# Performance work log

Measured on AMD Instinct MI355X. Metric: run time of the kernel, lower is better.

## Reference

```python
import jax, jax.numpy as jnp
import numpy as np

B, T, D, H, LORA = 4, 1024, 1024, 16, 64
HD = D // H
BLOCK_ID, N_BLOCKS = 6, 12


def _ln(x, w, b, eps=1e-5):
    m = x.mean(-1, keepdims=True)
    v = ((x - m) ** 2).mean(-1, keepdims=True)
    return (x - m) * jax.lax.rsqrt(v + eps) * w + b


def _lora(z, a, b, l):
    return l + jnp.tanh(z @ a.T) @ b.T


def setup_inputs() -> dict:
    key = jax.random.key(0)
    ks = iter(jax.random.split(key, 64))
    rn = lambda shape, s: jax.random.normal(next(ks), shape, jnp.float32) * s
    inp = {}
    inp['x'] = rn((B, T, D), 1.0)
    r1 = 1.0 - BLOCK_ID / N_BLOCKS
    i = np.arange(D)
    inp['xw'] = jnp.asarray(1.0 - (i / D) ** r1, jnp.float32)
    for nm in ('rW', 'kW', 'vW', 'gW'):
        inp[nm] = rn((D, D), 0.02)
    for p in ('r', 'k', 'v', 'g', 'd'):
        inp[p + '_la'] = rn((LORA, D), 0.001)
        inp[p + '_lb'] = rn((D, LORA), 0.001)
        inp[p + '_ll'] = rn((D,), 1.0)
    inp['ln_w'] = jnp.full((HD,), ((1 + BLOCK_ID) / N_BLOCKS) ** 0.7, jnp.float32)
    inp['ln_b'] = jnp.zeros((HD,), jnp.float32)
    inp['oW'] = rn((D, D), 0.02)
    inp['init_state'] = rn((H, HD, HD), 1.0)
    r0 = BLOCK_ID / (N_BLOCKS - 1)
    ih = i % HD
    inp['u'] = jnp.asarray(r0 * (1 - ih / (D - 1)) + np.remainder(0.1 * (ih + 1), 3.0), jnp.float32)
    return inp


def reference(x, xw, rW, kW, vW, gW, r_la, r_lb, r_ll, k_la, k_lb, k_ll,
              v_la, v_lb, v_ll, g_la, g_lb, g_ll, d_la, d_lb, d_ll,
              ln_w, ln_b, oW, init_state, u):
    b, t, d = x.shape
    h = init_state.shape[0]
    hd = d // h
    # token shift: xx[t] = x[t-1], xx[0] = 0
    xx = jnp.concatenate([jnp.zeros_like(x[:, :1]), x[:, :-1]], axis=1)
    dx = xx - x
    lerpx = x + dx * xw
    r = (x + dx * _lora(lerpx, r_la, r_lb, r_ll)) @ rW.T
    k = (x + dx * _lora(lerpx, k_la, k_lb, k_ll)) @ kW.T
    v = (x + dx * _lora(lerpx, v_la, v_lb, v_ll)) @ vW.T
    g = (x + dx * _lora(lerpx, g_la, g_lb, g_ll)) @ gW.T
    w = jnp.exp(-jnp.exp(_lora(x + dx * _lora(lerpx, d_la, d_lb, d_ll), d_la, d_lb, d_ll)))
    # [B,T,D] -> [T,B,H,hd] for the time scan
    split = lambda z: z.reshape(b, t, h, hd).transpose(1, 0, 2, 3)
    rs, ws, ks, vs = split(r), split(w), split(k), split(v)
    uh = u.reshape(h, hd)
    st0 = jnp.broadcast_to(init_state, (b, h, hd, hd))

    def step(st, inp):
        rt, wt, kt, vt = inp
        kv = jnp.einsum('bhi,bhj->bhij', kt, vt)      # outer product
        y = jnp.einsum('bhi,bhij->bhj', rt, st + uh[None, :, :, None] * kv)
        return wt[..., None] * st + kv, y             # diag(w) @ S + kv

    st1, ys = jax.lax.scan(step, st0, (rs, ws, ks, vs))  # ys: [T,B,H,hd]
    o = jax.nn.silu(g.reshape(b, t, h, hd)) * _ln(ys.transpose(1, 0, 2, 3), ln_w, ln_b)
    return o.reshape(b, t, d) @ oW.T, st1
```

## Files before the change

### kernel.cpp

```cpp
#include <hip/hip_runtime.h>
#include <hip/hip_bf16.h>

typedef unsigned short u16;
typedef unsigned int u32;
typedef __attribute__((ext_vector_type(2))) float f32x2;
typedef __attribute__((ext_vector_type(4))) float f32x4;
typedef __attribute__((ext_vector_type(4))) u32 u32x4;
typedef __attribute__((ext_vector_type(8))) short s16x8;

#define AS1 __attribute__((address_space(1)))
#define AS3 __attribute__((address_space(3)))

#define NB 4
#define TTOK 1024
#define DD 1024
#define NH 16
#define HD 64
#define MT 4096
#define NCH 16
#define CLEN 64

struct Ptr8 { u16* p[8]; };
struct CPtr8 { const u16* p[8]; };

static __device__ __forceinline__ float b2f(u16 u) {
  union { unsigned int u; float f; } c; c.u = ((unsigned int)u) << 16; return c.f;
}
static __device__ __forceinline__ float ubit(u32 u) {
  union { u32 u; float f; } c; c.u = u; return c.f;
}
static __device__ __forceinline__ u16 f2b(float f) {
  union { float f; unsigned int u; } c; c.f = f;
  return (u16)((c.u + 0x7fffu + ((c.u >> 16) & 1u)) >> 16);
}
static __device__ __forceinline__ void gload16(const u16* g, u16* l) {
  __builtin_amdgcn_global_load_lds((const AS1 u32*)g, (AS3 u32*)l, 16, 0, 0);
}
static __device__ __forceinline__ int swz(int lin) {
  return lin ^ (((lin >> 9) & 3) << 5) ^ (((lin >> 7) & 1) << 4);
}

__global__ __launch_bounds__(256) void convW(const float* __restrict__ s0, const float* __restrict__ s1,
                                             const float* __restrict__ s2, const float* __restrict__ s3,
                                             const float* __restrict__ s4, u16* __restrict__ dst) {
  long f = ((long)blockIdx.x * 256 + threadIdx.x) << 2;
  int sel = (int)(f >> 20);
  const float* s = sel == 0 ? s0 : sel == 1 ? s1 : sel == 2 ? s2 : sel == 3 ? s3 : s4;
  long off = f & 1048575;
  f32x4 v = *(const f32x4*)&s[off];
  ushort4 o; o.x = f2b(v[0]); o.y = f2b(v[1]); o.z = f2b(v[2]); o.w = f2b(v[3]);
  *(ushort4*)&dst[f] = o;
}

__global__ __launch_bounds__(256) void convLora(
    const float* a0, const float* a1, const float* a2, const float* a3, const float* a4,
    const float* b0, const float* b1, const float* b2, const float* b3, const float* b4,
    const float* l0, const float* l1, const float* l2, const float* l3, const float* l4,
    u16* __restrict__ laD, u16* __restrict__ lbD, float* __restrict__ llD) {
  long f = ((long)blockIdx.x * 256 + threadIdx.x) << 2;
  if (f < 327680) {
    int sel = (int)(f >> 16); long off = f & 65535;
    const float* s = sel == 0 ? a0 : sel == 1 ? a1 : sel == 2 ? a2 : sel == 3 ? a3 : a4;
    f32x4 v = *(const f32x4*)&s[off];
    ushort4 o; o.x = f2b(v[0]); o.y = f2b(v[1]); o.z = f2b(v[2]); o.w = f2b(v[3]);
    *(ushort4*)&laD[f] = o;
  } else if (f < 655360) {
    long g = f - 327680;
    int sel = (int)(g >> 16); long off = g & 65535;
    const float* s = sel == 0 ? b0 : sel == 1 ? b1 : sel == 2 ? b2 : sel == 3 ? b3 : b4;
    f32x4 v = *(const f32x4*)&s[off];
    ushort4 o; o.x = f2b(v[0]); o.y = f2b(v[1]); o.z = f2b(v[2]); o.w = f2b(v[3]);
    *(ushort4*)&lbD[g] = o;
  } else if (f < 660480) {
    long g = f - 655360;
    int sel = (int)(g >> 10); long off = g & 1023;
    const float* s = sel == 0 ? l0 : sel == 1 ? l1 : sel == 2 ? l2 : sel == 3 ? l3 : l4;
    *(f32x4*)&llD[g] = *(const f32x4*)&s[off];
  }
}

__global__ __launch_bounds__(256) void prep(const float* __restrict__ x, const float* __restrict__ xw,
                                            u16* __restrict__ lerpx, u16* __restrict__ xB,
                                            u16* __restrict__ dxB) {
  long f = ((long)blockIdx.x * 256 + threadIdx.x) << 2;
  int d = (int)(f & (DD - 1));
  int m = (int)(f >> 10);
  int t = m & (TTOK - 1);
  f32x4 xv = *(const f32x4*)&x[f];
  f32x4 xm = {};
  if (t > 0) xm = *(const f32x4*)&x[f - DD];
  f32x4 xwv = *(const f32x4*)&xw[d];
  f32x4 dx = xm - xv;
  f32x4 lp = xv + dx * xwv;
  ushort4 o; o.x = f2b(lp[0]); o.y = f2b(lp[1]); o.z = f2b(lp[2]); o.w = f2b(lp[3]);
  *(ushort4*)&lerpx[f] = o;
  ushort4 ox; ox.x = f2b(xv[0]); ox.y = f2b(xv[1]); ox.z = f2b(xv[2]); ox.w = f2b(xv[3]);
  *(ushort4*)&xB[f] = ox;
  ushort4 od; od.x = f2b(dx[0]); od.y = f2b(dx[1]); od.z = f2b(dx[2]); od.w = f2b(dx[3]);
  *(ushort4*)&dxB[f] = od;
}

template<int BM, int BN, int EPI>
__launch_bounds__(256)
__global__ void gemm2(const u16* __restrict__ Ab, long sAz,
                      const u16* __restrict__ Bb, long sBz,
                      void* __restrict__ Ob, long sOz,
                      const float* __restrict__ llb,
                      const u16* __restrict__ xB,
                      const u16* __restrict__ dxB,
                      int M, int N, int K) {
  __shared__ __align__(16) u16 As[BM * 64];
  __shared__ __align__(16) u16 Bs[BN * 64];
  const int z = blockIdx.z;
  const u16* A = Ab + (long)z * sAz;
  const u16* Bw = Bb + (long)z * sBz;
  const int m0 = blockIdx.x * BM;
  const int n0 = blockIdx.y * BN;
  const int tid = threadIdx.x;
  const int l = tid & 63;
  const int wv = tid >> 6;
  constexpr int WM = BM / 2, WN = BN / 2;
  constexpr int FM = WM / 16, FN = WN / 16;
  const int wm0 = (wv >> 1) * WM, wn0 = (wv & 1) * WN;
  const int lrow = l & 15, lk = (l >> 4) * 8;
  constexpr int GA = BM / 32, GB = BN / 32;
  int gA[GA], gB[GB];
#pragma unroll
  for (int q = 0; q < GA; ++q) {
    int d = (q * 256 + tid) * 16;
    int bb = swz(d);
    gA[q] = (m0 + (bb >> 7)) * K + ((bb & 127) >> 1);
  }
#pragma unroll
  for (int q = 0; q < GB; ++q) {
    int d = (q * 256 + tid) * 16;
    int bb = swz(d);
    gB[q] = (n0 + (bb >> 7)) * K + ((bb & 127) >> 1);
  }
  int aOff[FM][2], bOff[FN][2];
#pragma unroll
  for (int m = 0; m < FM; ++m)
#pragma unroll
    for (int kk = 0; kk < 2; ++kk)
      aOff[m][kk] = swz(((wm0 + m * 16 + lrow) << 7) + (kk << 6) + (lk << 1));
#pragma unroll
  for (int n = 0; n < FN; ++n)
#pragma unroll
    for (int kk = 0; kk < 2; ++kk)
      bOff[n][kk] = swz(((wn0 + n * 16 + lrow) << 7) + (kk << 6) + (lk << 1));
  f32x4 acc[FM][FN] = {};
  for (int k0 = 0; k0 < K; k0 += 64) {
    __syncthreads();
#pragma unroll
    for (int q = 0; q < GA; ++q)
      gload16(&A[(long)gA[q] + k0], (u16*)((char*)As + (q * 256 + tid) * 16));
#pragma unroll
    for (int q = 0; q < GB; ++q)
      gload16(&Bw[(long)gB[q] + k0], (u16*)((char*)Bs + (q * 256 + tid) * 16));
    __syncthreads();
#pragma unroll
    for (int kk = 0; kk < 2; ++kk) {
      s16x8 af[FM], bfr[FN];
#pragma unroll
      for (int m = 0; m < FM; ++m) af[m] = *(const s16x8*)((const char*)As + aOff[m][kk]);
#pragma unroll
      for (int n = 0; n < FN; ++n) bfr[n] = *(const s16x8*)((const char*)Bs + bOff[n][kk]);
#pragma unroll
      for (int m = 0; m < FM; ++m)
#pragma unroll
        for (int n = 0; n < FN; ++n)
          acc[m][n] = __builtin_amdgcn_mfma_f32_16x16x32_bf16(af[m], bfr[n], acc[m][n], 0, 0, 0);
    }
  }
#pragma unroll
  for (int m = 0; m < FM; ++m) {
#pragma unroll
    for (int n = 0; n < FN; ++n) {
      const int j = n0 + wn0 + n * 16 + lrow;
#pragma unroll
      for (int q = 0; q < 4; ++q) {
        const int i = m0 + wm0 + m * 16 + (l >> 4) * 4 + q;
        const long off = (long)i * N + j;
        float v = acc[m][n][q];
        if constexpr (EPI == 0) {
          ((float*)Ob + (long)z * sOz)[off] = v;
        } else if constexpr (EPI == 1) {
          ((u16*)Ob + (long)z * sOz)[off] = f2b(tanhf(v));
        } else if constexpr (EPI == 2) {
          float val = b2f(xB[off]) + b2f(dxB[off]) * (llb[(long)z * N + j] + v);
          ((u16*)Ob + (long)z * sOz)[off] = f2b(val);
        } else if constexpr (EPI == 3) {
          ((float*)Ob + (long)z * sOz)[off] = expf(-expf(llb[j] + v));
        } else {
          ((u16*)Ob + (long)z * sOz)[off] = f2b(v);
        }
      }
    }
  }
}

__global__ __launch_bounds__(512) void scan_local(
    const u16* __restrict__ rP, const u16* __restrict__ kP,
    const u16* __restrict__ vP, const float* __restrict__ wP,
    const float* __restrict__ uP, Ptr8 YS,
    u16* __restrict__ rtil, float* __restrict__ SL, float* __restrict__ AC) {
  __shared__ __align__(16) u16 Rs[64 * 64];
  __shared__ __align__(16) u16 Ks[64 * 64];
  __shared__ __align__(16) u16 Vs[64 * 64];
  __shared__ __align__(16) float Ws[64 * 64];
  const int bhc = blockIdx.x;
  const int c = bhc & (NCH - 1), h = (bhc >> 4) & (NH - 1), b = bhc >> 8;
  const int tid = threadIdx.x;
  const int j = tid & 63;
  const int qu = tid >> 6;
  const long base0 = ((long)(b * TTOK + c * CLEN) << 10) + h * HD;
  {
    int t = tid >> 3, off = (tid & 7) * 8;
    gload16(&rP[base0 + (long)t * DD + off], (u16*)Rs + tid * 8);
    gload16(&kP[base0 + (long)t * DD + off], (u16*)Ks + tid * 8);
    gload16(&vP[base0 + (long)t * DD + off], (u16*)Vs + tid * 8);
  }
#pragma unroll
  for (int q = 0; q < 2; ++q) {
    int cidx = q * 512 + tid;
    int t = cidx >> 4, off = (cidx & 15) * 4;
    __builtin_amdgcn_global_load_lds((const AS1 u32*)&wP[base0 + (long)t * DD + off],
                                     (AS3 u32*)((float*)Ws + cidx * 4), 16, 0, 0);
  }
  __syncthreads();
  const int so = qu * 8;
  f32x2 s2[4] = {};
  float Aj = 1.f;
  const float uj = (qu == 1) ? uP[h * HD + j] : 0.f;
  long base = base0;
  u16* __restrict__ ysel =
      qu == 0 ? YS.p[0] : qu == 1 ? YS.p[1] : qu == 2 ? YS.p[2] : qu == 3 ? YS.p[3] :
      qu == 4 ? YS.p[4] : qu == 5 ? YS.p[5] : qu == 6 ? YS.p[6] : YS.p[7];
  for (int tt = 0; tt < CLEN; ++tt) {
    const int ro = tt * 64 + so;
    u32x4 ra = *(const u32x4*)&Rs[ro];
    u32x4 ka = *(const u32x4*)&Ks[ro];
    f32x2 wv2[4];
#pragma unroll
    for (int e = 0; e < 4; ++e) wv2[e] = *(const f32x2*)&Ws[ro + 2 * e];
    const float vj = b2f(Vs[tt * 64 + j]);
    const f32x2 vj2 = {vj, vj};
    f32x2 y2 = {0.f, 0.f};
#pragma unroll
    for (int e = 0; e < 4; ++e) {
      const u32 pr = ra[e], pk = ka[e];
      f32x2 r01; r01[0] = ubit(pr << 16); r01[1] = ubit(pr & 0xffff0000u);
      f32x2 k01; k01[0] = ubit(pk << 16); k01[1] = ubit(pk & 0xffff0000u);
      y2 = __builtin_elementwise_fma(r01, s2[e], y2);
      s2[e] = __builtin_elementwise_fma(wv2[e], s2[e], k01 * vj2);
    }
    float y = y2[0] + y2[1];
    if (qu == 0) {
      const float rj = b2f(Rs[tt * 64 + j]);
      const float wj = Ws[tt * 64 + j];
      rtil[base + j] = f2b(rj * Aj);
      Aj *= wj;
    } else if (qu == 1) {
      const float rj = b2f(Rs[tt * 64 + j]);
      const float kj = b2f(Ks[tt * 64 + j]);
      float al = rj * uj * kj;
#pragma unroll
      for (int msk = 1; msk < 64; msk <<= 1) al += __shfl_xor(al, msk, 64);
      y = fmaf(al, vj, y);
    }
    ysel[base + j] = f2b(y);
    base += DD;
  }
#pragma unroll
  for (int e = 0; e < 4; ++e) {
    SL[((long)bhc * 64 + so + 2 * e) * 64 + j] = s2[e][0];
    SL[((long)bhc * 64 + so + 2 * e + 1) * 64 + j] = s2[e][1];
  }
  if (qu == 0) AC[(long)bhc * 64 + j] = Aj;
}

__global__ __launch_bounds__(256) void scan_prop(
    float* __restrict__ SL, const float* __restrict__ AC,
    const float* __restrict__ initS, float* __restrict__ st1) {
  const int bh = blockIdx.x >> 2;
  const int jq = blockIdx.x & 3;
  const int h = bh & (NH - 1);
  const int i = threadIdx.x >> 2;
  const int jo = jq * 16 + (threadIdx.x & 3) * 4;
  f32x4 sin4 = *(const f32x4*)(initS + ((long)h * 64 + i) * 64 + jo);
  for (int cc = 0; cc < NCH; ++cc) {
    const long bhc = (long)bh * NCH + cc;
    f32x4* slp = (f32x4*)(SL + (bhc * 64 + i) * 64 + jo);
    const float Ai = AC[bhc * 64 + i];
    f32x4 sl = *slp;
    *slp = sin4;
    sin4 = Ai * sin4 + sl;
  }
  *(f32x4*)(st1 + ((long)bh * 64 + i) * 64 + jo) = sin4;
}

__global__ __launch_bounds__(256) void scan_corr(
    const float* __restrict__ SL, const u16* __restrict__ rtil, float* __restrict__ ysC) {
  __shared__ __align__(16) float S[64 * 64];
  const int bhc = blockIdx.x;
  const int c = bhc & (NCH - 1), h = (bhc >> 4) & (NH - 1), b = bhc >> 8;
  const int tid = threadIdx.x;
  const f32x4* sp = (const f32x4*)(SL + (long)bhc * 4096);
  for (int q = tid; q < 1024; q += 256) ((f32x4*)S)[q] = sp[q];
  __syncthreads();
  const int t = tid >> 2, jg = (tid & 3) * 16;
  const long base = ((long)(b * TTOK + c * CLEN + t) * DD) + h * HD;
  f32x4 yacc[4] = {};
  const u16* rp = rtil + base;
#pragma unroll 8
  for (int i = 0; i < 64; ++i) {
    const float r = b2f(rp[i]);
    const f32x4* srow = (const f32x4*)&S[i * 64 + jg];
#pragma unroll
    for (int e = 0; e < 4; ++e) yacc[e] += r * srow[e];
  }
  f32x4* yp = (f32x4*)(ysC + base + jg);
#pragma unroll
  for (int e = 0; e < 4; ++e) yp[e] = yacc[e];
}

__global__ __launch_bounds__(256) void ln_silu(
    CPtr8 P, const float* __restrict__ ysC,
    const u16* __restrict__ gP,
    const float* __restrict__ lnw, const float* __restrict__ lnb,
    u16* __restrict__ oB) {
  const int ridx = blockIdx.x * 4 + (threadIdx.x >> 6);
  const int lane = threadIdx.x & 63;
  const long basem = (long)ridx * 64;
  float y = ysC[basem + lane];
#pragma unroll
  for (int q = 0; q < 8; ++q) y += b2f(P.p[q][basem + lane]);
  float su = y, sq = y * y;
#pragma unroll
  for (int msk = 1; msk < 64; msk <<= 1) {
    su += __shfl_xor(su, msk, 64);
    sq += __shfl_xor(sq, msk, 64);
  }
  const float mean = su * (1.f / 64.f);
  const float var = sq * (1.f / 64.f) - mean * mean;
  const float rs = rsqrtf(var + 1e-5f);
  const float g = b2f(gP[basem + lane]);
  const float silu = g / (1.f + expf(-g));
  const float val = silu * ((y - mean) * rs * lnw[lane] + lnb[lane]);
  oB[basem + lane] = f2b(val);
}

extern "C" void kernel_launch(void* const* d_in, const int* in_sizes, int n_in,
                              void* d_out, int out_size, void* d_ws, size_t ws_size,
                              hipStream_t stream) {
  const float* x   = (const float*)d_in[0];
  const float* xw  = (const float*)d_in[1];
  const float* rW  = (const float*)d_in[2];
  const float* kW  = (const float*)d_in[3];
  const float* vW  = (const float*)d_in[4];
  const float* gW  = (const float*)d_in[5];
  const float* r_la = (const float*)d_in[6],  *r_lb = (const float*)d_in[7],  *r_ll = (const float*)d_in[8];
  const float* k_la = (const float*)d_in[9],  *k_lb = (const float*)d_in[10], *k_ll = (const float*)d_in[11];
  const float* v_la = (const float*)d_in[12], *v_lb = (const float*)d_in[13], *v_ll = (const float*)d_in[14];
  const float* g_la = (const float*)d_in[15], *g_lb = (const float*)d_in[16], *g_ll = (const float*)d_in[17];
  const float* d_la = (const float*)d_in[18], *d_lb = (const float*)d_in[19], *d_ll = (const float*)d_in[20];
  const float* lnw = (const float*)d_in[21];
  const float* lnb = (const float*)d_in[22];
  const float* oW  = (const float*)d_in[23];
  const float* initS = (const float*)d_in[24];
  const float* uP  = (const float*)d_in[25];
  float* out = (float*)d_out;

  char* ws = (char*)d_ws;
  u16*   W_all  = (u16*)(ws + 0);
  u16*   la_all = (u16*)(ws + 10485760);
  u16*   lb_all = (u16*)(ws + 11141120);
  float* ll_all = (float*)(ws + 11796480);
  u16*   lerpx  = (u16*)(ws + 11816960);
  u16*   xB     = (u16*)(ws + 20205568);
  u16*   dxB    = (u16*)(ws + 28594176);
  u16*   t1_all = (u16*)(ws + 36982784);
  u16*   z_all  = (u16*)(ws + 39604224);
  u16*   rkvg   = (u16*)(ws + 81547264);
  float* wbuf   = (float*)(ws + 115101696);
  u16*   rtil   = (u16*)(ws + 131878912);
  float* SL     = (float*)(ws + 140267520);
  float* AC     = (float*)(ws + 157044736);
  u16*   ys0p   = (u16*)(ws + 157306880);
  u16*   oB     = (u16*)(ws + 174084096);
  float* ysC    = (float*)(ws + 115101696);

  Ptr8 YS;
  YS.p[0] = ys0p;
  YS.p[1] = (u16*)(ws + 11816960);
  YS.p[2] = (u16*)(ws + 20205568);
  YS.p[3] = (u16*)(ws + 28594176);
  YS.p[4] = (u16*)(ws + 39604224);
  YS.p[5] = (u16*)(ws + 47992832);
  YS.p[6] = (u16*)(ws + 56381440);
  YS.p[7] = (u16*)(ws + 64770048);

  convW<<<5120, 256, 0, stream>>>(rW, kW, vW, gW, oW, W_all);
  convLora<<<645, 256, 0, stream>>>(r_la, k_la, v_la, g_la, d_la,
                                    r_lb, k_lb, v_lb, g_lb, d_lb,
                                    r_ll, k_ll, v_ll, g_ll, d_ll,
                                    la_all, lb_all, ll_all);
  prep<<<4096, 256, 0, stream>>>(x, xw, lerpx, xB, dxB);

  gemm2<64, 64, 1><<<dim3(64, 1, 5), 256, 0, stream>>>(
      lerpx, 0L, la_all, 65536L, (void*)t1_all, 262144L, nullptr, nullptr, nullptr, MT, 64, 1024);
  gemm2<128, 128, 2><<<dim3(32, 8, 5), 256, 0, stream>>>(
      t1_all, 262144L, lb_all, 65536L, (void*)z_all, 4194304L, ll_all, xB, dxB, MT, 1024, 64);
  gemm2<64, 64, 1><<<dim3(64, 1, 1), 256, 0, stream>>>(
      z_all + 4L * 4194304, 0L, la_all + 4L * 65536, 0L, (void*)t1_all, 0L, nullptr, nullptr, nullptr, MT, 64, 1024);
  gemm2<128, 128, 3><<<dim3(32, 8, 1), 256, 0, stream>>>(
      t1_all, 0L, lb_all + 4L * 65536, 0L, (void*)wbuf, 0L, ll_all + 4096, nullptr, nullptr, MT, 1024, 64);
  gemm2<128, 128, 4><<<dim3(32, 8, 4), 256, 0, stream>>>(
      z_all, 4194304L, W_all, 1048576L, (void*)rkvg, 4194304L, nullptr, nullptr, nullptr, MT, 1024, 1024);

  scan_local<<<1024, 512, 0, stream>>>(rkvg, rkvg + 4194304L, rkvg + 2L * 4194304, wbuf,
                                       uP, YS, rtil, SL, AC);
  scan_prop<<<256, 256, 0, stream>>>(SL, AC, initS, out + 4194304);
  scan_corr<<<1024, 256, 0, stream>>>(SL, rtil, ysC);

  CPtr8 YSc;
  for (int q = 0; q < 8; ++q) YSc.p[q] = YS.p[q];
  ln_silu<<<16384, 256, 0, stream>>>(YSc, ysC, rkvg + 3L * 4194304, lnw, lnb, oB);
  gemm2<128, 128, 0><<<dim3(32, 8, 1), 256, 0, stream>>>(
      oB, 0L, W_all + 4L * 1048576, 0L, (void*)out, 0L, nullptr, nullptr, nullptr, MT, 1024, 1024);
}
```

Before: 352.4 us.

## Reduce scan partial outputs in LDS instead of eight global bf16 buffers

In the intra-chunk scan, each of the eight row-slice wavegroups now adds its partial y into a shared fp32 tile with LDS atomics, and the block writes one bf16 output tile. Previously each wrote its own bf16 partial buffer to global memory. This removes seven global partial writes and seven reads in the LN/SiLU kernel. R and K are also converted to fp32 once when loaded into LDS, which drops per-step bf16 unpacking. The cost is LDS atomic contention in the inner time loop, plus a larger LDS footprint that may lower occupancy.

```diff
diff --git a/kernel.cpp b/kernel.cpp
--- a/kernel.cpp
+++ b/kernel.cpp
@@ -20,14 +20,8 @@
 #define NCH 16
 #define CLEN 64
 
-struct Ptr8 { u16* p[8]; };
-struct CPtr8 { const u16* p[8]; };
-
 static __device__ __forceinline__ float b2f(u16 u) {
   union { unsigned int u; float f; } c; c.u = ((unsigned int)u) << 16; return c.f;
-}
-static __device__ __forceinline__ float ubit(u32 u) {
-  union { u32 u; float f; } c; c.u = u; return c.f;
 }
 static __device__ __forceinline__ u16 f2b(float f) {
   union { float f; unsigned int u; } c; c.f = f;
@@ -202,30 +196,41 @@
 __global__ __launch_bounds__(512) void scan_local(
     const u16* __restrict__ rP, const u16* __restrict__ kP,
     const u16* __restrict__ vP, const float* __restrict__ wP,
-    const float* __restrict__ uP, Ptr8 YS,
+    const float* __restrict__ uP, u16* __restrict__ ysB,
     u16* __restrict__ rtil, float* __restrict__ SL, float* __restrict__ AC) {
-  __shared__ __align__(16) u16 Rs[64 * 64];
-  __shared__ __align__(16) u16 Ks[64 * 64];
+  __shared__ __align__(16) float Rf[64 * 64];
+  __shared__ __align__(16) float Kf[64 * 64];
+  __shared__ __align__(16) float Wf[64 * 64];
+  __shared__ __align__(16) float Ys[64 * 64];
   __shared__ __align__(16) u16 Vs[64 * 64];
-  __shared__ __align__(16) float Ws[64 * 64];
   const int bhc = blockIdx.x;
   const int c = bhc & (NCH - 1), h = (bhc >> 4) & (NH - 1), b = bhc >> 8;
   const int tid = threadIdx.x;
   const int j = tid & 63;
   const int qu = tid >> 6;
   const long base0 = ((long)(b * TTOK + c * CLEN) << 10) + h * HD;
-  {
-    int t = tid >> 3, off = (tid & 7) * 8;
-    gload16(&rP[base0 + (long)t * DD + off], (u16*)Rs + tid * 8);
-    gload16(&kP[base0 + (long)t * DD + off], (u16*)Ks + tid * 8);
-    gload16(&vP[base0 + (long)t * DD + off], (u16*)Vs + tid * 8);
-  }
+  const int st = tid >> 3, sjo = (tid & 7) * 8;
+  gload16(&vP[base0 + (long)st * DD + sjo], (u16*)Vs + tid * 8);
 #pragma unroll
   for (int q = 0; q < 2; ++q) {
     int cidx = q * 512 + tid;
     int t = cidx >> 4, off = (cidx & 15) * 4;
     __builtin_amdgcn_global_load_lds((const AS1 u32*)&wP[base0 + (long)t * DD + off],
-                                     (AS3 u32*)((float*)Ws + cidx * 4), 16, 0, 0);
+                                     (AS3 u32*)((float*)Wf + cidx * 4), 16, 0, 0);
+  }
+  {
+    s16x8 rv = *(const s16x8*)&rP[base0 + (long)st * DD + sjo];
+    s16x8 kv = *(const s16x8*)&kP[base0 + (long)st * DD + sjo];
+    f32x4 r0, r1, k0, k1;
+#pragma unroll
+    for (int e = 0; e < 4; ++e) {
+      r0[e] = b2f((u16)rv[e]); r1[e] = b2f((u16)rv[e + 4]);
+      k0[e] = b2f((u16)kv[e]); k1[e] = b2f((u16)kv[e + 4]);
+    }
+    *(f32x4*)&Rf[st * 64 + sjo] = r0; *(f32x4*)&Rf[st * 64 + sjo + 4] = r1;
+    *(f32x4*)&Kf[st * 64 + sjo] = k0; *(f32x4*)&Kf[st * 64 + sjo + 4] = k1;
+    f32x4 zz = {};
+    *(f32x4*)&Ys[tid * 8] = zz; *(f32x4*)&Ys[tid * 8 + 4] = zz;
   }
   __syncthreads();
   const int so = qu * 8;
@@ -233,42 +238,51 @@
   float Aj = 1.f;
   const float uj = (qu == 1) ? uP[h * HD + j] : 0.f;
   long base = base0;
-  u16* __restrict__ ysel =
-      qu == 0 ? YS.p[0] : qu == 1 ? YS.p[1] : qu == 2 ? YS.p[2] : qu == 3 ? YS.p[3] :
-      qu == 4 ? YS.p[4] : qu == 5 ? YS.p[5] : qu == 6 ? YS.p[6] : YS.p[7];
   for (int tt = 0; tt < CLEN; ++tt) {
     const int ro = tt * 64 + so;
-    u32x4 ra = *(const u32x4*)&Rs[ro];
-    u32x4 ka = *(const u32x4*)&Ks[ro];
-    f32x2 wv2[4];
-#pragma unroll
-    for (int e = 0; e < 4; ++e) wv2[e] = *(const f32x2*)&Ws[ro + 2 * e];
+    const f32x4 r03 = *(const f32x4*)&Rf[ro];
+    const f32x4 r47 = *(const f32x4*)&Rf[ro + 4];
+    const f32x4 k03 = *(const f32x4*)&Kf[ro];
+    const f32x4 k47 = *(const f32x4*)&Kf[ro + 4];
+    const f32x4 w03 = *(const f32x4*)&Wf[ro];
+    const f32x4 w47 = *(const f32x4*)&Wf[ro + 4];
     const float vj = b2f(Vs[tt * 64 + j]);
     const f32x2 vj2 = {vj, vj};
     f32x2 y2 = {0.f, 0.f};
-#pragma unroll
-    for (int e = 0; e < 4; ++e) {
-      const u32 pr = ra[e], pk = ka[e];
-      f32x2 r01; r01[0] = ubit(pr << 16); r01[1] = ubit(pr & 0xffff0000u);
-      f32x2 k01; k01[0] = ubit(pk << 16); k01[1] = ubit(pk & 0xffff0000u);
-      y2 = __builtin_elementwise_fma(r01, s2[e], y2);
-      s2[e] = __builtin_elementwise_fma(wv2[e], s2[e], k01 * vj2);
+    {
+      const f32x2 rp = {r03[0], r03[1]}, kp = {k03[0], k03[1]}, wp = {w03[0], w03[1]};
+      y2 = __builtin_elementwise_fma(rp, s2[0], y2);
+      s2[0] = __builtin_elementwise_fma(wp, s2[0], kp * vj2);
+    }
+    {
+      const f32x2 rp = {r03[2], r03[3]}, kp = {k03[2], k03[3]}, wp = {w03[2], w03[3]};
+      y2 = __builtin_elementwise_fma(rp, s2[1], y2);
+      s2[1] = __builtin_elementwise_fma(wp, s2[1], kp * vj2);
+    }
+    {
+      const f32x2 rp = {r47[0], r47[1]}, kp = {k47[0], k47[1]}, wp = {w47[0], w47[1]};
+      y2 = __builtin_elementwise_fma(rp, s2[2], y2);
+      s2[2] = __builtin_elementwise_fma(wp, s2[2], kp * vj2);
+    }
+    {
+      const f32x2 rp = {r47[2], r47[3]}, kp = {k47[2], k47[3]}, wp = {w47[2], w47[3]};
+      y2 = __builtin_elementwise_fma(rp, s2[3], y2);
+      s2[3] = __builtin_elementwise_fma(wp, s2[3], kp * vj2);
     }
     float y = y2[0] + y2[1];
     if (qu == 0) {
-      const float rj = b2f(Rs[tt * 64 + j]);
-      const float wj = Ws[tt * 64 + j];
+      const float rj = Rf[tt * 64 + j];
       rtil[base + j] = f2b(rj * Aj);
-      Aj *= wj;
+      Aj *= Wf[tt * 64 + j];
     } else if (qu == 1) {
-      const float rj = b2f(Rs[tt * 64 + j]);
-      const float kj = b2f(Ks[tt * 64 + j]);
+      const float rj = Rf[tt * 64 + j];
+      const float kj = Kf[tt * 64 + j];
       float al = rj * uj * kj;
 #pragma unroll
       for (int msk = 1; msk < 64; msk <<= 1) al += __shfl_xor(al, msk, 64);
       y = fmaf(al, vj, y);
     }
-    ysel[base + j] = f2b(y);
+    atomicAdd(&Ys[tt * 64 + j], y);
     base += DD;
   }
 #pragma unroll
@@ -277,6 +291,15 @@
     SL[((long)bhc * 64 + so + 2 * e + 1) * 64 + j] = s2[e][1];
   }
   if (qu == 0) AC[(long)bhc * 64 + j] = Aj;
+  __syncthreads();
+  {
+    const f32x4 a = *(const f32x4*)&Ys[st * 64 + sjo];
+    const f32x4 bq = *(const f32x4*)&Ys[st * 64 + sjo + 4];
+    s16x8 o;
+#pragma unroll
+    for (int e = 0; e < 4; ++e) { o[e] = (short)f2b(a[e]); o[e + 4] = (short)f2b(bq[e]); }
+    *(s16x8*)&ysB[base0 + (long)st * DD + sjo] = o;
+  }
 }
 
 __global__ __launch_bounds__(256) void scan_prop(
@@ -325,16 +348,14 @@
 }
 
 __global__ __launch_bounds__(256) void ln_silu(
-    CPtr8 P, const float* __restrict__ ysC,
+    const u16* __restrict__ ysB, const float* __restrict__ ysC,
     const u16* __restrict__ gP,
     const float* __restrict__ lnw, const float* __restrict__ lnb,
     u16* __restrict__ oB) {
   const int ridx = blockIdx.x * 4 + (threadIdx.x >> 6);
   const int lane = threadIdx.x & 63;
   const long basem = (long)ridx * 64;
-  float y = ysC[basem + lane];
-#pragma unroll
-  for (int q = 0; q < 8; ++q) y += b2f(P.p[q][basem + lane]);
+  const float y = b2f(ysB[basem + lane]) + ysC[basem + lane];
   float su = y, sq = y * y;
 #pragma unroll
   for (int msk = 1; msk < 64; msk <<= 1) {
@@ -386,19 +407,9 @@
   u16*   rtil   = (u16*)(ws + 131878912);
   float* SL     = (float*)(ws + 140267520);
   float* AC     = (float*)(ws + 157044736);
-  u16*   ys0p   = (u16*)(ws + 157306880);
+  u16*   ysB    = (u16*)(ws + 157306880);
   u16*   oB     = (u16*)(ws + 174084096);
   float* ysC    = (float*)(ws + 115101696);
-
-  Ptr8 YS;
-  YS.p[0] = ys0p;
-  YS.p[1] = (u16*)(ws + 11816960);
-  YS.p[2] = (u16*)(ws + 20205568);
-  YS.p[3] = (u16*)(ws + 28594176);
-  YS.p[4] = (u16*)(ws + 39604224);
-  YS.p[5] = (u16*)(ws + 47992832);
-  YS.p[6] = (u16*)(ws + 56381440);
-  YS.p[7] = (u16*)(ws + 64770048);
 
   convW<<<5120, 256, 0, stream>>>(rW, kW, vW, gW, oW, W_all);
   convLora<<<645, 256, 0, stream>>>(r_la, k_la, v_la, g_la, d_la,
@@ -419,13 +430,11 @@
       z_all, 4194304L, W_all, 1048576L, (void*)rkvg, 4194304L, nullptr, nullptr, nullptr, MT, 1024, 1024);
 
   scan_local<<<1024, 512, 0, stream>>>(rkvg, rkvg + 4194304L, rkvg + 2L * 4194304, wbuf,
-                                       uP, YS, rtil, SL, AC);
+                                       uP, ysB, rtil, SL, AC);
   scan_prop<<<256, 256, 0, stream>>>(SL, AC, initS, out + 4194304);
   scan_corr<<<1024, 256, 0, stream>>>(SL, rtil, ysC);
 
-  CPtr8 YSc;
-  for (int q = 0; q < 8; ++q) YSc.p[q] = YS.p[q];
-  ln_silu<<<16384, 256, 0, stream>>>(YSc, ysC, rkvg + 3L * 4194304, lnw, lnb, oB);
+  ln_silu<<<16384, 256, 0, stream>>>(ysB, ysC, rkvg + 3L * 4194304, lnw, lnb, oB);
   gemm2<128, 128, 0><<<dim3(32, 8, 1), 256, 0, stream>>>(
       oB, 0L, W_all + 4L * 1048576, 0L, (void*)out, 0L, nullptr, nullptr, nullptr, MT, 1024, 1024);
 }
```

Result: slower. 513.4 us (+45.7%).
